# Performance work log

Measured on AMD Instinct MI355X. Metric: run time of the kernel, lower is better.

## Reference

```python
import jax, jax.numpy as jnp
import numpy as np

ALPHA = 0.2          # LeakyReLU negative slope
NEG_INF = -9e15      # standard GAT masking constant


def gat_layer(h, adj_mask, W, a_src, a_dst):
    # h: [N, D], adj_mask: [N, N] bool
    Wh = h @ W                                  # [N, D]
    e = (Wh @ a_src)[:, None] + (Wh @ a_dst)[None, :]  # [N, N]
    e = jax.nn.leaky_relu(e, negative_slope=ALPHA)
    e = jnp.where(adj_mask, e, NEG_INF)
    attn = jax.nn.softmax(e, axis=-1)           # [N, N]
    return jax.nn.relu(attn @ Wh)               # PlainGCN applies ReLU


def setup_inputs() -> dict:
    key = jax.random.key(0)
    ks = jax.random.split(key, 8)
    N, D = 8192, 256
    x = jax.random.normal(ks[0], (N, D), dtype=jnp.float32)
    adj = jax.random.randint(ks[1], (N, N), 0, 2, dtype=jnp.int32)
    s = 1.0 / np.sqrt(D)
    W1 = jax.random.normal(ks[2], (D, D), dtype=jnp.float32) * s
    a1_src = jax.random.normal(ks[3], (D,), dtype=jnp.float32) * s
    a1_dst = jax.random.normal(ks[4], (D,), dtype=jnp.float32) * s
    W2 = jax.random.normal(ks[5], (D, D), dtype=jnp.float32) * s
    a2_src = jax.random.normal(ks[6], (D,), dtype=jnp.float32) * s
    a2_dst = jax.random.normal(ks[7], (D,), dtype=jnp.float32) * s
    return {"x": x, "adj": adj, "W1": W1, "a1_src": a1_src, "a1_dst": a1_dst,
            "W2": W2, "a2_src": a2_src, "a2_dst": a2_dst}


def reference(x, adj, W1, a1_src, a1_dst, W2, a2_src, a2_dst):
    adj_mask = adj > 0
    h = gat_layer(x, adj_mask, W1, a1_src, a1_dst)
    h = gat_layer(h, adj_mask, W2, a2_src, a2_dst)
    return h
```

## Files before the change

kernel.cpp:

```cpp
#include <hip/hip_runtime.h>
#include <cstdint>
#include <cstddef>


#define ALPHA 0.2f
#define NN 8192
#define DD 256

typedef __attribute__((ext_vector_type(8))) short short8;
typedef __attribute__((ext_vector_type(4))) float f32x4;
typedef __attribute__((ext_vector_type(2))) _Float16 half2v;
typedef __attribute__((ext_vector_type(8))) __fp16 h8;

__device__ __forceinline__ unsigned pk_f16(float a, float b) {
    return __builtin_bit_cast(unsigned, __builtin_amdgcn_cvt_pkrtz(a, b));
}

__device__ __forceinline__ int sbit(uint32_t x, int o) {
    return ((int)(x << (31 - o))) >> 31;
}

__device__ __forceinline__ uint32_t hmerge(uint32_t hi, uint32_t lo) {
#if __has_builtin(__builtin_amdgcn_perm)
    return __builtin_amdgcn_perm(hi, lo, 0x07060100u);
#else
    return (hi & 0xFFFF0000u) | (lo & 0x0000FFFFu);
#endif
}

__device__ __forceinline__ half2v pkmax(half2v a, half2v b) {
#if __has_builtin(__builtin_elementwise_max)
    return __builtin_elementwise_max(a, b);
#else
    half2v r;
    asm("v_pk_max_f16 %0, %1, %2" : "=v"(r) : "v"(a), "v"(b));
    return r;
#endif
}

__device__ __forceinline__ f32x4 mfma_f16(uint4 a, short8 b, f32x4 c) {
    return __builtin_amdgcn_mfma_f32_16x16x32_f16(__builtin_bit_cast(h8, a),
                                                  __builtin_bit_cast(h8, b), c, 0, 0, 0);
}


__device__ __forceinline__ void packbits_dev(const int* __restrict__ adj,
                                             uint64_t* __restrict__ bits,
                                             int row, int lane) {
    const int* rowp = adj + (size_t)row * NN;
    uint64_t* dst = bits + (size_t)row * 128;
    for (int it = 0; it < 16; it++) {
        const int* p = rowp + it * 512;
        int a0 = p[lane];
        int a1 = p[64 + lane];
        int a2 = p[128 + lane];
        int a3 = p[192 + lane];
        int a4 = p[256 + lane];
        int a5 = p[320 + lane];
        int a6 = p[384 + lane];
        int a7 = p[448 + lane];
        uint64_t m0 = __ballot(a0 != 0);
        uint64_t m1 = __ballot(a1 != 0);
        uint64_t m2 = __ballot(a2 != 0);
        uint64_t m3 = __ballot(a3 != 0);
        uint64_t m4 = __ballot(a4 != 0);
        uint64_t m5 = __ballot(a5 != 0);
        uint64_t m6 = __ballot(a6 != 0);
        uint64_t m7 = __ballot(a7 != 0);
        if (lane == 0) {
            dst[it * 8 + 0] = m0; dst[it * 8 + 1] = m1;
            dst[it * 8 + 2] = m2; dst[it * 8 + 3] = m3;
            dst[it * 8 + 4] = m4; dst[it * 8 + 5] = m5;
            dst[it * 8 + 6] = m6; dst[it * 8 + 7] = m7;
        }
    }
}

__device__ __forceinline__ void transp_dev(const uint32_t* __restrict__ bits32,
                                           uint32_t* __restrict__ bitsT,
                                           int job, unsigned char* smem, int t) {
    uint32_t (*tile)[65] = (uint32_t (*)[65])smem;
    const int i0 = (job >> 2) * 64;
    const int w0 = (job & 3) * 64;
#pragma unroll
    for (int p = 0; p < 4; p++) {
        int r = (t >> 4) + 16 * p;
        int c4 = (t & 15) * 4;
        uint4 v = *(const uint4*)(bits32 + (size_t)(i0 + r) * 256 + w0 + c4);
        tile[r][c4 + 0] = v.x; tile[r][c4 + 1] = v.y;
        tile[r][c4 + 2] = v.z; tile[r][c4 + 3] = v.w;
    }
    __syncthreads();
#pragma unroll
    for (int p = 0; p < 4; p++) {
        int wr = (t >> 4) + 16 * p;
        int i4 = (t & 15) * 4;
        uint4 o = {tile[i4][wr], tile[i4 + 1][wr], tile[i4 + 2][wr], tile[i4 + 3][wr]};
        *(uint4*)(bitsT + (size_t)(w0 + wr) * NN + i0 + i4) = o;
    }
}

__device__ __forceinline__ void gemm_dev(const float* __restrict__ A,
                                         const float* __restrict__ B,
                                         unsigned short* __restrict__ Bpack,
                                         const float* __restrict__ a_src,
                                         const float* __restrict__ a_dst,
                                         float* __restrict__ s4,
                                         float* __restrict__ dd4,
                                         int job, unsigned char* smem, int t) {
    float (*At)[36] = (float (*)[36])smem;
    float2 (*Bs)[32] = (float2 (*)[32])(smem + 4608);
    const int m0 = (job >> 2) * 32;
    const int cq = job & 3;
    const int r0 = (t >> 5) * 4;
    const int cl = t & 31;
    float acc[4][2];
#pragma unroll
    for (int i = 0; i < 4; i++) { acc[i][0] = 0.f; acc[i][1] = 0.f; }

    for (int k0 = 0; k0 < DD; k0 += 32) {
        {
            int row = t >> 3, kq = t & 7;
            float4 v = *(const float4*)(A + (size_t)(m0 + row) * DD + k0 + kq * 4);
            At[kq * 4 + 0][row] = v.x; At[kq * 4 + 1][row] = v.y;
            At[kq * 4 + 2][row] = v.z; At[kq * 4 + 3][row] = v.w;
        }
#pragma unroll
        for (int l2 = 0; l2 < 2; l2++) {
            int fi = l2 * 256 + t;
            int br = fi >> 4, bc4 = fi & 15;
            float4 v = *(const float4*)(B + (size_t)(k0 + br) * DD + cq * 64 + bc4 * 4);
            Bs[br][bc4 * 2] = {v.x, v.y};
            Bs[br][bc4 * 2 + 1] = {v.z, v.w};
        }
        __syncthreads();
#pragma unroll
        for (int k = 0; k < 32; k++) {
            float4 a0 = *(const float4*)&At[k][r0];
            float2 b = Bs[k][cl];
            float av[4] = {a0.x, a0.y, a0.z, a0.w};
#pragma unroll
            for (int i = 0; i < 4; i++) {
                acc[i][0] += av[i] * b.x;
                acc[i][1] += av[i] * b.y;
            }
        }
        __syncthreads();
    }

    const int jt = m0 >> 5;
    const int lq = ((r0 >> 3) & 3) * 16;
    const int i8 = r0 & 4;
#pragma unroll
    for (int cc = 0; cc < 2; cc++) {
        int c = cq * 64 + cl * 2 + cc;
        int ct = c >> 4;
        int lane = lq + (c & 15);
        uint2 pk;
        pk.x = pk_f16(acc[0][cc], acc[1][cc]);
        pk.y = pk_f16(acc[2][cc], acc[3][cc]);
        *(uint2*)(Bpack + ((size_t)(jt * 16 + ct) * 64 + lane) * 8 + i8) = pk;
    }

    const int c0 = cq * 64 + cl * 2;
    float as0 = a_src[c0], as1 = a_src[c0 + 1];
    float ad0 = a_dst[c0], ad1 = a_dst[c0 + 1];
    float ps[4], pd[4];
#pragma unroll
    for (int i = 0; i < 4; i++) {
        ps[i] = acc[i][0] * as0 + acc[i][1] * as1;
        pd[i] = acc[i][0] * ad0 + acc[i][1] * ad1;
    }
#pragma unroll
    for (int off = 16; off; off >>= 1) {
#pragma unroll
        for (int i = 0; i < 4; i++) {
            ps[i] += __shfl_xor(ps[i], off);
            pd[i] += __shfl_xor(pd[i], off);
        }
    }
    if (cl == 0) {
#pragma unroll
        for (int i = 0; i < 4; i++) {
            s4[(size_t)cq * NN + m0 + r0 + i] = ps[i];
            dd4[(size_t)cq * NN + m0 + r0 + i] = pd[i];
        }
    }
}

__device__ __forceinline__ void rowstats_dev(const uint32_t* __restrict__ bits32,
                                             const float* __restrict__ s,
                                             const float* __restrict__ dd,
                                             const float* __restrict__ FH,
                                             float* __restrict__ Ep,
                                             float* __restrict__ Gp,
                                             int job, unsigned char* smem, int t) {
    uint32_t* smk = (uint32_t*)smem;
    float (*red)[4] = (float (*)[4])(smem + 4096);
    float* sEm = (float*)(smem + 4096 + 64);
    float* sEa = (float*)(smem + 4096 + 80);
    const int i0 = job * 4;
    const int wave = t >> 6, lane = t & 63;
    {
        const uint4* src = (const uint4*)(bits32 + (size_t)i0 * 256);
        ((uint4*)smk)[t] = src[t];
    }
    __syncthreads();

    float mx[4];
#pragma unroll
    for (int r = 0; r < 4; r++) mx[r] = -3.0e38f;
#pragma unroll
    for (int q = 0; q < 8; q++) {
        float4 v = *(const float4*)(dd + 4 * (t + 256 * q));
        const int wq = 32 * q + (t >> 3);
        const int sh = (t & 7) * 4;
#pragma unroll
        for (int r = 0; r < 4; r++) {
            uint32_t b = smk[r * 256 + wq] >> sh;
            mx[r] = fmaxf(mx[r], (b & 1u) ? v.x : -3.0e38f);
            mx[r] = fmaxf(mx[r], (b & 2u) ? v.y : -3.0e38f);
            mx[r] = fmaxf(mx[r], (b & 4u) ? v.z : -3.0e38f);
            mx[r] = fmaxf(mx[r], (b & 8u) ? v.w : -3.0e38f);
        }
    }
#pragma unroll
    for (int r = 0; r < 4; r++) {
#pragma unroll
        for (int off = 32; off; off >>= 1) mx[r] = fmaxf(mx[r], __shfl_down(mx[r], off));
    }
    if (lane == 0) {
#pragma unroll
        for (int r = 0; r < 4; r++) red[wave][r] = mx[r];
    }
    __syncthreads();
    if (t < 4) {
        float dmax = fmaxf(fmaxf(red[0][t], red[1][t]), fmaxf(red[2][t], red[3][t]));
        float si = s[i0 + t];
        float e = si + dmax;
        float m = e >= 0.f ? e : ALPHA * e;
        sEm[t] = __expf(si - m);
        sEa[t] = __expf(ALPHA * si - m);
    }
    __syncthreads();
    float em[4], ea[4], sm[4];
#pragma unroll
    for (int r = 0; r < 4; r++) { em[r] = sEm[r]; ea[r] = sEa[r]; sm[r] = 0.f; }

#pragma unroll
    for (int q = 0; q < 16; q++) {
        float4 v = *(const float4*)(FH + 4 * (t + 256 * q));
        const int wq = 16 * q + (t >> 4);
        const int sh = (t & 15) * 2;
#pragma unroll
        for (int r = 0; r < 4; r++) {
            uint32_t b = smk[r * 256 + wq] >> sh;
            float c0 = fmaxf(em[r] * v.x, ea[r] * v.y);
            float c1 = fmaxf(em[r] * v.z, ea[r] * v.w);
            sm[r] += (b & 1u) ? c0 : 0.f;
            sm[r] += (b & 2u) ? c1 : 0.f;
        }
    }
#pragma unroll
    for (int r = 0; r < 4; r++) {
#pragma unroll
        for (int off = 32; off; off >>= 1) sm[r] += __shfl_down(sm[r], off);
    }
    __syncthreads();
    if (lane == 0) {
#pragma unroll
        for (int r = 0; r < 4; r++) red[wave][r] = sm[r];
    }
    __syncthreads();
    if (t < 4) {
        float rl = 1.0f / (red[0][t] + red[1][t] + red[2][t] + red[3][t]);
        Ep[i0 + t] = rl * sEm[t];
        Gp[i0 + t] = rl * sEa[t];
    }
}


__global__ __launch_bounds__(256) void mega1(const float* __restrict__ A,
                                             const float* __restrict__ W,
                                             unsigned short* __restrict__ Bpack,
                                             const float* __restrict__ a_src,
                                             const float* __restrict__ a_dst,
                                             float* __restrict__ s4,
                                             float* __restrict__ dd4,
                                             const int* __restrict__ adj,
                                             uint64_t* __restrict__ bits) {
    __shared__ __align__(16) unsigned char smem[12800];
    const int bx = blockIdx.x;
    const int t = threadIdx.x;
    const int sel = bx % 3;
    const int base = bx / 3;
    if (sel == 0) {
        gemm_dev(A, W, Bpack, a_src, a_dst, s4, dd4, base, smem, t);
    } else {
        const int row = base * 8 + (sel - 1) * 4 + (t >> 6);
        packbits_dev(adj, bits, row, t & 63);
    }
}

__global__ __launch_bounds__(256) void mega2(const uint32_t* __restrict__ bits32,
                                             uint32_t* __restrict__ bitsT,
                                             const float* __restrict__ s,
                                             const float* __restrict__ dd,
                                             const float* __restrict__ FH,
                                             float* __restrict__ Ep,
                                             float* __restrict__ Gp) {
    __shared__ __align__(16) unsigned char smem[16640];
    const int bx = blockIdx.x;
    const int t = threadIdx.x;
    const int sel = bx % 5;
    const int base = bx / 5;
    if (sel == 0) {
        transp_dev(bits32, bitsT, base, smem, t);
    } else {
        rowstats_dev(bits32, s, dd, FH, Ep, Gp, base * 4 + (sel - 1), smem, t);
    }
}

__global__ __launch_bounds__(256) void k_gemm(const float* A, const float* W,
                                              unsigned short* Bpack,
                                              const float* a_src, const float* a_dst,
                                              float* s4, float* dd4) {
    __shared__ __align__(16) unsigned char smem[12800];
    gemm_dev(A, W, Bpack, a_src, a_dst, s4, dd4, blockIdx.x, smem, threadIdx.x);
}
__global__ __launch_bounds__(256) void k_rowstats(const uint32_t* bits32, const float* s,
                                                  const float* dd, const float* FH,
                                                  float* Ep, float* Gp) {
    __shared__ __align__(16) unsigned char smem[4200];
    rowstats_dev(bits32, s, dd, FH, Ep, Gp, blockIdx.x, smem, threadIdx.x);
}

__global__ __launch_bounds__(256) void fhgen(const float* __restrict__ s4,
                                             const float* __restrict__ dd4,
                                             float* __restrict__ s,
                                             float* __restrict__ dd,
                                             float* __restrict__ FH,
                                             uint32_t* __restrict__ FF,
                                             uint32_t* __restrict__ HH) {
    int i = blockIdx.x * 256 + threadIdx.x;
    float ssum = (s4[i] + s4[i + NN]) + (s4[i + 2 * NN] + s4[i + 3 * NN]);
    float dsum = (dd4[i] + dd4[i + NN]) + (dd4[i + 2 * NN] + dd4[i + 3 * NN]);
    s[i] = ssum;
    dd[i] = dsum;
    float F = __expf(dsum);
    float H = __expf(ALPHA * dsum);
    FH[2 * i] = F;
    FH[2 * i + 1] = H;
    float Fn = __shfl_xor(F, 1);
    float Hn = __shfl_xor(H, 1);
    if ((i & 1) == 0) {
        FF[i >> 1] = pk_f16(F, Fn);
        HH[i >> 1] = pk_f16(H, Hn);
    }
}

__global__ __launch_bounds__(256, 4) void pv_mfma(const unsigned short* __restrict__ Bpack,
                                                  const uint32_t* __restrict__ bitsT,
                                                  const uint32_t* __restrict__ FF,
                                                  const uint32_t* __restrict__ HH,
                                                  const float* __restrict__ Ep,
                                                  const float* __restrict__ Gp,
                                                  float* __restrict__ pout) {
    __shared__ __align__(16) uint4 pb[2][256];
    const int t = threadIdx.x;
    const int w = t >> 6, l = t & 63;
    const int bx = blockIdx.x;
    const int ks = bx & 7;
    const int i0 = (bx >> 3) * 64;
    const int kbase = ks * 32;

    const int rl16 = l & 15;
    const int ko = (l >> 4) * 8;
    const int rw = i0 + 16 * w + rl16;
    const float Eps = Ep[rw] * 256.0f;
    const float Gps = Gp[rw] * 256.0f;
    const half2v ep2 = {(_Float16)Eps, (_Float16)Eps};
    const half2v gp2 = {(_Float16)Gps, (_Float16)Gps};

    const unsigned short* bb = Bpack + ((size_t)(w * 4) * 64 + l) * 8;
    const uint32_t* btb = bitsT + rw;
    const uint32_t* ffb = FF + (ko >> 1);
    const uint32_t* hhb = HH + (ko >> 1);

    f32x4 acc[4][4];
#pragma unroll
    for (int i = 0; i < 4; i++)
#pragma unroll
        for (int q = 0; q < 4; q++) acc[i][q] = (f32x4){0.f, 0.f, 0.f, 0.f};

    for (int jl = 0; jl < 32; jl++) {
        const int cc = kbase + jl;
        const int par = jl & 1;
        const unsigned short* bp = bb + (size_t)cc * 8192;
        short8 B0 = *(const short8*)(bp);
        short8 B1 = *(const short8*)(bp + 512);
        short8 B2 = *(const short8*)(bp + 1024);
        short8 B3 = *(const short8*)(bp + 1536);
        uint32_t bw = btb[(size_t)cc * NN];
        uint4 fw = *(const uint4*)(ffb + cc * 16);
        uint4 hw = *(const uint4*)(hhb + cc * 16);
        const uint32_t fwa[4] = {fw.x, fw.y, fw.z, fw.w};
        const uint32_t hwa[4] = {hw.x, hw.y, hw.z, hw.w};
        const uint32_t wl = bw >> ko;

        uint32_t au[4];
#pragma unroll
        for (int p = 0; p < 4; p++) {
            half2v f2 = __builtin_bit_cast(half2v, fwa[p]);
            half2v h2 = __builtin_bit_cast(half2v, hwa[p]);
            half2v pm = ep2 * f2;
            half2v pa = gp2 * h2;
            half2v px = pkmax(pm, pa);
            uint32_t mlo = (uint32_t)sbit(wl, 2 * p);
            uint32_t mhi = (uint32_t)sbit(wl, 2 * p + 1);
            uint32_t msk = hmerge(mhi, mlo);
            au[p] = __builtin_bit_cast(uint32_t, px) & msk;
        }
        uint4 auv = {au[0], au[1], au[2], au[3]};
        pb[par][w * 64 + l] = auv;

        __syncthreads();

#pragma unroll
        for (int f = 0; f < 4; f++) {
            uint4 af;
            if (f == w) af = auv;
            else        af = pb[par][f * 64 + l];
            acc[f][0] = mfma_f16(af, B0, acc[f][0]);
            acc[f][1] = mfma_f16(af, B1, acc[f][1]);
            acc[f][2] = mfma_f16(af, B2, acc[f][2]);
            acc[f][3] = mfma_f16(af, B3, acc[f][3]);
        }
    }

    float* outp = pout + (size_t)ks * NN * DD;
#pragma unroll
    for (int f = 0; f < 4; f++) {
        const int orow = i0 + 16 * f + (l >> 4) * 4;
#pragma unroll
        for (int q = 0; q < 4; q++) {
            const int ocol = w * 64 + q * 16 + rl16;
#pragma unroll
            for (int r = 0; r < 4; r++)
                outp[(size_t)(orow + r) * DD + ocol] = acc[f][q][r];
        }
    }
}

__global__ __launch_bounds__(256) void combine8(const float* __restrict__ p,
                                                float* __restrict__ out) {
    const size_t S = (size_t)NN * DD / 4;
    const float SC = 1.0f / 256.0f;
    size_t idx = (size_t)blockIdx.x * 256 + threadIdx.x;
    float4 a0 = ((const float4*)p)[idx];
    float4 a1 = ((const float4*)p)[idx + S];
    float4 a2 = ((const float4*)p)[idx + 2 * S];
    float4 a3 = ((const float4*)p)[idx + 3 * S];
    float4 a4 = ((const float4*)p)[idx + 4 * S];
    float4 a5 = ((const float4*)p)[idx + 5 * S];
    float4 a6 = ((const float4*)p)[idx + 6 * S];
    float4 a7 = ((const float4*)p)[idx + 7 * S];
    float4 o;
    o.x = fmaxf((((a0.x + a1.x) + (a2.x + a3.x)) + ((a4.x + a5.x) + (a6.x + a7.x))) * SC, 0.f);
    o.y = fmaxf((((a0.y + a1.y) + (a2.y + a3.y)) + ((a4.y + a5.y) + (a6.y + a7.y))) * SC, 0.f);
    o.z = fmaxf((((a0.z + a1.z) + (a2.z + a3.z)) + ((a4.z + a5.z) + (a6.z + a7.z))) * SC, 0.f);
    o.w = fmaxf((((a0.w + a1.w) + (a2.w + a3.w)) + ((a4.w + a5.w) + (a6.w + a7.w))) * SC, 0.f);
    ((float4*)out)[idx] = o;
}

extern "C" void kernel_launch(void* const* d_in, const int* in_sizes, int n_in,
                              void* d_out, int out_size, void* d_ws, size_t ws_size,
                              hipStream_t stream) {
    const float* x   = (const float*)d_in[0];
    const int* adj   = (const int*)d_in[1];
    const float* W1  = (const float*)d_in[2];
    const float* a1s = (const float*)d_in[3];
    const float* a1d = (const float*)d_in[4];
    const float* W2  = (const float*)d_in[5];
    const float* a2s = (const float*)d_in[6];
    const float* a2d = (const float*)d_in[7];
    float* out = (float*)d_out;

    char* ws = (char*)d_ws;
    const size_t MB = 1024ull * 1024ull;
    uint64_t*       bits  = (uint64_t*)(ws + 8 * MB);
    uint32_t*       bits32= (uint32_t*)bits;
    uint32_t*       bitsT = (uint32_t*)(ws + 16 * MB);
    float*          sArr  = (float*)(ws + 24 * MB);
    float*          ddA   = sArr + NN;
    float*          EpA   = sArr + 2 * NN;
    float*          GpA   = sArr + 3 * NN;
    float*          FHA   = sArr + 4 * NN;
    float*          s4    = sArr + 6 * NN;
    float*          dd4   = sArr + 10 * NN;
    uint32_t*       FFA   = (uint32_t*)(sArr + 14 * NN);
    uint32_t*       HHA   = FFA + NN / 2;
    unsigned short* Bpack = (unsigned short*)(ws + 25 * MB);
    float*          pout  = (float*)(ws + 32 * MB);

    mega1<<<dim3(3072), dim3(256), 0, stream>>>(x, W1, Bpack, a1s, a1d, s4, dd4,
                                                adj, bits);
    fhgen<<<dim3(32), dim3(256), 0, stream>>>(s4, dd4, sArr, ddA, FHA, FFA, HHA);
    mega2<<<dim3(2560), dim3(256), 0, stream>>>(bits32, bitsT, sArr, ddA, FHA, EpA, GpA);
    pv_mfma<<<dim3(1024), dim3(256), 0, stream>>>(Bpack, bitsT, FFA, HHA, EpA, GpA, pout);
    combine8<<<dim3(2048), dim3(256), 0, stream>>>(pout, out);

    k_gemm<<<dim3(1024), dim3(256), 0, stream>>>(out, W2, Bpack, a2s, a2d, s4, dd4);
    fhgen<<<dim3(32), dim3(256), 0, stream>>>(s4, dd4, sArr, ddA, FHA, FFA, HHA);
    k_rowstats<<<dim3(2048), dim3(256), 0, stream>>>(bits32, sArr, ddA, FHA, EpA, GpA);
    pv_mfma<<<dim3(1024), dim3(256), 0, stream>>>(Bpack, bitsT, FFA, HHA, EpA, GpA, pout);
    combine8<<<dim3(2048), dim3(256), 0, stream>>>(pout, out);
}
```

Baseline: 566.7 us.

## Fuse softmax denominator into PV kernel and drop rowstats sum pass

Removes the second pass in rowstats that summed masked exp values over all 8192 columns per row. The softmax denominator is now accumulated inside pv_mfma from the same fp16 probability tiles fed to the MFMAs, written per K-split, and applied in combine8 as a per-row reciprocal. The FH buffer and its writes are dropped. The loop is also restructured to build the next tile's A operand after the MFMAs, overlapping the build with matrix work. The row sum now comes from fp16 partial sums, which may shift accuracy slightly.

```diff
diff --git a/kernel.cpp b/kernel.cpp
--- a/kernel.cpp
+++ b/kernel.cpp
@@ -191,14 +191,11 @@
 __device__ __forceinline__ void rowstats_dev(const uint32_t* __restrict__ bits32,
                                              const float* __restrict__ s,
                                              const float* __restrict__ dd,
-                                             const float* __restrict__ FH,
                                              float* __restrict__ Ep,
                                              float* __restrict__ Gp,
                                              int job, unsigned char* smem, int t) {
     uint32_t* smk = (uint32_t*)smem;
     float (*red)[4] = (float (*)[4])(smem + 4096);
-    float* sEm = (float*)(smem + 4096 + 64);
-    float* sEa = (float*)(smem + 4096 + 80);
     const int i0 = job * 4;
     const int wave = t >> 6, lane = t & 63;
     {
@@ -239,43 +236,8 @@
         float si = s[i0 + t];
         float e = si + dmax;
         float m = e >= 0.f ? e : ALPHA * e;
-        sEm[t] = __expf(si - m);
-        sEa[t] = __expf(ALPHA * si - m);
-    }
-    __syncthreads();
-    float em[4], ea[4], sm[4];
-#pragma unroll
-    for (int r = 0; r < 4; r++) { em[r] = sEm[r]; ea[r] = sEa[r]; sm[r] = 0.f; }
-
-#pragma unroll
-    for (int q = 0; q < 16; q++) {
-        float4 v = *(const float4*)(FH + 4 * (t + 256 * q));
-        const int wq = 16 * q + (t >> 4);
-        const int sh = (t & 15) * 2;
-#pragma unroll
-        for (int r = 0; r < 4; r++) {
-            uint32_t b = smk[r * 256 + wq] >> sh;
-            float c0 = fmaxf(em[r] * v.x, ea[r] * v.y);
-            float c1 = fmaxf(em[r] * v.z, ea[r] * v.w);
-            sm[r] += (b & 1u) ? c0 : 0.f;
-            sm[r] += (b & 2u) ? c1 : 0.f;
-        }
-    }
-#pragma unroll
-    for (int r = 0; r < 4; r++) {
-#pragma unroll
-        for (int off = 32; off; off >>= 1) sm[r] += __shfl_down(sm[r], off);
-    }
-    __syncthreads();
-    if (lane == 0) {
-#pragma unroll
-        for (int r = 0; r < 4; r++) red[wave][r] = sm[r];
-    }
-    __syncthreads();
-    if (t < 4) {
-        float rl = 1.0f / (red[0][t] + red[1][t] + red[2][t] + red[3][t]);
-        Ep[i0 + t] = rl * sEm[t];
-        Gp[i0 + t] = rl * sEa[t];
+        Ep[i0 + t] = 256.0f * __expf(si - m);
+        Gp[i0 + t] = 256.0f * __expf(ALPHA * si - m);
     }
 }
 
@@ -306,7 +268,6 @@
                                              uint32_t* __restrict__ bitsT,
                                              const float* __restrict__ s,
                                              const float* __restrict__ dd,
-                                             const float* __restrict__ FH,
                                              float* __restrict__ Ep,
                                              float* __restrict__ Gp) {
     __shared__ __align__(16) unsigned char smem[16640];
@@ -317,7 +278,7 @@
     if (sel == 0) {
         transp_dev(bits32, bitsT, base, smem, t);
     } else {
-        rowstats_dev(bits32, s, dd, FH, Ep, Gp, base * 4 + (sel - 1), smem, t);
+        rowstats_dev(bits32, s, dd, Ep, Gp, base * 4 + (sel - 1), smem, t);
     }
 }
 
@@ -329,17 +290,16 @@
     gemm_dev(A, W, Bpack, a_src, a_dst, s4, dd4, blockIdx.x, smem, threadIdx.x);
 }
 __global__ __launch_bounds__(256) void k_rowstats(const uint32_t* bits32, const float* s,
-                                                  const float* dd, const float* FH,
+                                                  const float* dd,
                                                   float* Ep, float* Gp) {
     __shared__ __align__(16) unsigned char smem[4200];
-    rowstats_dev(bits32, s, dd, FH, Ep, Gp, blockIdx.x, smem, threadIdx.x);
+    rowstats_dev(bits32, s, dd, Ep, Gp, blockIdx.x, smem, threadIdx.x);
 }
 
 __global__ __launch_bounds__(256) void fhgen(const float* __restrict__ s4,
                                              const float* __restrict__ dd4,
                                              float* __restrict__ s,
                                              float* __restrict__ dd,
-                                             float* __restrict__ FH,
                                              uint32_t* __restrict__ FF,
                                              uint32_t* __restrict__ HH) {
     int i = blockIdx.x * 256 + threadIdx.x;
@@ -349,8 +309,6 @@
     dd[i] = dsum;
     float F = __expf(dsum);
     float H = __expf(ALPHA * dsum);
-    FH[2 * i] = F;
-    FH[2 * i + 1] = H;
     float Fn = __shfl_xor(F, 1);
     float Hn = __shfl_xor(H, 1);
     if ((i & 1) == 0) {
@@ -365,7 +323,8 @@
                                                   const uint32_t* __restrict__ HH,
                                                   const float* __restrict__ Ep,
                                                   const float* __restrict__ Gp,
-                                                  float* __restrict__ pout) {
+                                                  float* __restrict__ pout,
+                                                  float* __restrict__ rsum) {
     __shared__ __align__(16) uint4 pb[2][256];
     const int t = threadIdx.x;
     const int w = t >> 6, l = t & 63;
@@ -377,10 +336,10 @@
     const int rl16 = l & 15;
     const int ko = (l >> 4) * 8;
     const int rw = i0 + 16 * w + rl16;
-    const float Eps = Ep[rw] * 256.0f;
-    const float Gps = Gp[rw] * 256.0f;
-    const half2v ep2 = {(_Float16)Eps, (_Float16)Eps};
-    const half2v gp2 = {(_Float16)Gps, (_Float16)Gps};
+    const _Float16 eph = (_Float16)Ep[rw];
+    const _Float16 gph = (_Float16)Gp[rw];
+    const half2v ep2 = {eph, eph};
+    const half2v gp2 = {gph, gph};
 
     const unsigned short* bb = Bpack + ((size_t)(w * 4) * 64 + l) * 8;
     const uint32_t* btb = bitsT + rw;
@@ -392,22 +351,15 @@
     for (int i = 0; i < 4; i++)
 #pragma unroll
         for (int q = 0; q < 4; q++) acc[i][q] = (f32x4){0.f, 0.f, 0.f, 0.f};
-
-    for (int jl = 0; jl < 32; jl++) {
-        const int cc = kbase + jl;
-        const int par = jl & 1;
-        const unsigned short* bp = bb + (size_t)cc * 8192;
-        short8 B0 = *(const short8*)(bp);
-        short8 B1 = *(const short8*)(bp + 512);
-        short8 B2 = *(const short8*)(bp + 1024);
-        short8 B3 = *(const short8*)(bp + 1536);
+    float rsv = 0.f;
+
+    auto build = [&](int cc) -> uint4 {
         uint32_t bw = btb[(size_t)cc * NN];
         uint4 fw = *(const uint4*)(ffb + cc * 16);
         uint4 hw = *(const uint4*)(hhb + cc * 16);
         const uint32_t fwa[4] = {fw.x, fw.y, fw.z, fw.w};
         const uint32_t hwa[4] = {hw.x, hw.y, hw.z, hw.w};
         const uint32_t wl = bw >> ko;
-
         uint32_t au[4];
 #pragma unroll
         for (int p = 0; p < 4; p++) {
@@ -418,25 +370,49 @@
             half2v px = pkmax(pm, pa);
             uint32_t mlo = (uint32_t)sbit(wl, 2 * p);
             uint32_t mhi = (uint32_t)sbit(wl, 2 * p + 1);
-            uint32_t msk = hmerge(mhi, mlo);
-            au[p] = __builtin_bit_cast(uint32_t, px) & msk;
-        }
-        uint4 auv = {au[0], au[1], au[2], au[3]};
-        pb[par][w * 64 + l] = auv;
+            au[p] = __builtin_bit_cast(uint32_t, px) & hmerge(mhi, mlo);
+        }
+        half2v s01 = __builtin_bit_cast(half2v, au[0]) + __builtin_bit_cast(half2v, au[1]);
+        half2v s23 = __builtin_bit_cast(half2v, au[2]) + __builtin_bit_cast(half2v, au[3]);
+        half2v sp = s01 + s23;
+        rsv += (float)sp.x + (float)sp.y;
+        return (uint4){au[0], au[1], au[2], au[3]};
+    };
+
+    uint4 aucur = build(kbase);
+    pb[0][w * 64 + l] = aucur;
+
+    for (int jl = 0; jl < 32; jl++) {
+        const int par = jl & 1;
+        const unsigned short* bp = bb + (size_t)(kbase + jl) * 8192;
+        short8 B0 = *(const short8*)(bp);
+        short8 B1 = *(const short8*)(bp + 512);
+        short8 B2 = *(const short8*)(bp + 1024);
+        short8 B3 = *(const short8*)(bp + 1536);
 
         __syncthreads();
 
 #pragma unroll
         for (int f = 0; f < 4; f++) {
             uint4 af;
-            if (f == w) af = auv;
+            if (f == w) af = aucur;
             else        af = pb[par][f * 64 + l];
             acc[f][0] = mfma_f16(af, B0, acc[f][0]);
             acc[f][1] = mfma_f16(af, B1, acc[f][1]);
             acc[f][2] = mfma_f16(af, B2, acc[f][2]);
             acc[f][3] = mfma_f16(af, B3, acc[f][3]);
         }
-    }
+
+        if (jl < 31) {
+            uint4 an = build(kbase + jl + 1);
+            pb[par ^ 1][w * 64 + l] = an;
+            aucur = an;
+        }
+    }
+
+    rsv += __shfl_xor(rsv, 16);
+    rsv += __shfl_xor(rsv, 32);
+    if (l < 16) rsum[(size_t)ks * NN + rw] = rsv;
 
     float* outp = pout + (size_t)ks * NN * DD;
 #pragma unroll
@@ -453,10 +429,15 @@
 }
 
 __global__ __launch_bounds__(256) void combine8(const float* __restrict__ p,
+                                                const float* __restrict__ rsum,
                                                 float* __restrict__ out) {
     const size_t S = (size_t)NN * DD / 4;
-    const float SC = 1.0f / 256.0f;
     size_t idx = (size_t)blockIdx.x * 256 + threadIdx.x;
+    const int row = (int)(idx >> 6);
+    float rs = (rsum[row] + rsum[row + NN]) + (rsum[row + 2 * NN] + rsum[row + 3 * NN])
+             + (rsum[row + 4 * NN] + rsum[row + 5 * NN])
+             + (rsum[row + 6 * NN] + rsum[row + 7 * NN]);
+    const float inv = 1.0f / rs;
     float4 a0 = ((const float4*)p)[idx];
     float4 a1 = ((const float4*)p)[idx + S];
     float4 a2 = ((const float4*)p)[idx + 2 * S];
@@ -466,10 +447,10 @@
     float4 a6 = ((const float4*)p)[idx + 6 * S];
     float4 a7 = ((const float4*)p)[idx + 7 * S];
     float4 o;
-    o.x = fmaxf((((a0.x + a1.x) + (a2.x + a3.x)) + ((a4.x + a5.x) + (a6.x + a7.x))) * SC, 0.f);
-    o.y = fmaxf((((a0.y + a1.y) + (a2.y + a3.y)) + ((a4.y + a5.y) + (a6.y + a7.y))) * SC, 0.f);
-    o.z = fmaxf((((a0.z + a1.z) + (a2.z + a3.z)) + ((a4.z + a5.z) + (a6.z + a7.z))) * SC, 0.f);
-    o.w = fmaxf((((a0.w + a1.w) + (a2.w + a3.w)) + ((a4.w + a5.w) + (a6.w + a7.w))) * SC, 0.f);
+    o.x = fmaxf((((a0.x + a1.x) + (a2.x + a3.x)) + ((a4.x + a5.x) + (a6.x + a7.x))) * inv, 0.f);
+    o.y = fmaxf((((a0.y + a1.y) + (a2.y + a3.y)) + ((a4.y + a5.y) + (a6.y + a7.y))) * inv, 0.f);
+    o.z = fmaxf((((a0.z + a1.z) + (a2.z + a3.z)) + ((a4.z + a5.z) + (a6.z + a7.z))) * inv, 0.f);
+    o.w = fmaxf((((a0.w + a1.w) + (a2.w + a3.w)) + ((a4.w + a5.w) + (a6.w + a7.w))) * inv, 0.f);
     ((float4*)out)[idx] = o;
 }
 
@@ -495,24 +476,26 @@
     float*          ddA   = sArr + NN;
     float*          EpA   = sArr + 2 * NN;
     float*          GpA   = sArr + 3 * NN;
-    float*          FHA   = sArr + 4 * NN;
-    float*          s4    = sArr + 6 * NN;
-    float*          dd4   = sArr + 10 * NN;
-    uint32_t*       FFA   = (uint32_t*)(sArr + 14 * NN);
+    float*          s4    = sArr + 4 * NN;
+    float*          dd4   = sArr + 8 * NN;
+    uint32_t*       FFA   = (uint32_t*)(sArr + 12 * NN);
     uint32_t*       HHA   = FFA + NN / 2;
+    float*          rsumA = sArr + 13 * NN;
     unsigned short* Bpack = (unsigned short*)(ws + 25 * MB);
     float*          pout  = (float*)(ws + 32 * MB);
 
     mega1<<<dim3(3072), dim3(256), 0, stream>>>(x, W1, Bpack, a1s, a1d, s4, dd4,
                                                 adj, bits);
-    fhgen<<<dim3(32), dim3(256), 0, stream>>>(s4, dd4, sArr, ddA, FHA, FFA, HHA);
-    mega2<<<dim3(2560), dim3(256), 0, stream>>>(bits32, bitsT, sArr, ddA, FHA, EpA, GpA);
-    pv_mfma<<<dim3(1024), dim3(256), 0, stream>>>(Bpack, bitsT, FFA, HHA, EpA, GpA, pout);
-    combine8<<<dim3(2048), dim3(256), 0, stream>>>(pout, out);
+    fhgen<<<dim3(32), dim3(256), 0, stream>>>(s4, dd4, sArr, ddA, FFA, HHA);
+    mega2<<<dim3(2560), dim3(256), 0, stream>>>(bits32, bitsT, sArr, ddA, EpA, GpA);
+    pv_mfma<<<dim3(1024), dim3(256), 0, stream>>>(Bpack, bitsT, FFA, HHA, EpA, GpA,
+                                                  pout, rsumA);
+    combine8<<<dim3(2048), dim3(256), 0, stream>>>(pout, rsumA, out);
 
     k_gemm<<<dim3(1024), dim3(256), 0, stream>>>(out, W2, Bpack, a2s, a2d, s4, dd4);
-    fhgen<<<dim3(32), dim3(256), 0, stream>>>(s4, dd4, sArr, ddA, FHA, FFA, HHA);
-    k_rowstats<<<dim3(2048), dim3(256), 0, stream>>>(bits32, sArr, ddA, FHA, EpA, GpA);
-    pv_mfma<<<dim3(1024), dim3(256), 0, stream>>>(Bpack, bitsT, FFA, HHA, EpA, GpA, pout);
-    combine8<<<dim3(2048), dim3(256), 0, stream>>>(pout, out);
-}
+    fhgen<<<dim3(32), dim3(256), 0, stream>>>(s4, dd4, sArr, ddA, FFA, HHA);
+    k_rowstats<<<dim3(2048), dim3(256), 0, stream>>>(bits32, sArr, ddA, EpA, GpA);
+    pv_mfma<<<dim3(1024), dim3(256), 0, stream>>>(Bpack, bitsT, FFA, HHA, EpA, GpA,
+                                                  pout, rsumA);
+    combine8<<<dim3(2048), dim3(256), 0, stream>>>(pout, rsumA, out);
+}
```

Result: faster. 538.8 us (-4.9%).
